# Performance work log

Hardware: AMD Instinct MI355X
Metric: run time of the kernel (lower is better)

## Reference

```python
import jax, jax.numpy as jnp
import numpy as np

N, A, MO, LX, H, S, P, B, BL = 64, 128, 126, 96, 1024, 32, 2, 16, 32
T = (B - 2) * BL
L = B * BL        # 512
IN = MO + A + LX + S      # 382: cat([mo, aud, lxm, style])
GIN = IN + H              # 1406: GRU input = cat([in_embed, mo, aud, lxm, style])

def gelu(x):
    return jax.nn.gelu(x, approximate=False)  # torch F.gelu default (erf)

def gru_cell(x, h, wih, whh, bih, bhh):
    # torch nn.GRU cell math
    gi = x @ wih + bih  # [N,3H]
    gh = h @ whh + bhh  # [N,3H]
    ir, iz, inn = jnp.split(gi, 3, axis=-1)
    hr, hz, hn = jnp.split(gh, 3, axis=-1)
    r = jax.nn.sigmoid(ir + hr)
    z = jax.nn.sigmoid(iz + hz)
    n = jnp.tanh(inn + r * hn)
    return (1.0 - z) * n + z * h

def layernorm(x, g, b, eps=1e-5):
    m = x.mean(-1, keepdims=True)
    v = x.var(-1, keepdims=True)
    return (x - m) * jax.lax.rsqrt(v + eps) * g + b

def setup_inputs():
    key = jax.random.key(0)
    k = jax.random.split(key, 20)
    f = jnp.float32
    def rn(i, shape, s=0.05):
        return jax.random.normal(k[i], shape, dtype=f) * s
    return dict(
        aud_embed=jax.random.normal(k[0], (N, A, T), f),
        mo=jax.random.normal(k[1], (N, MO, L), f),
        lxm=jax.random.normal(k[2], (N, LX, B), f),
        vid_indices=jax.random.randint(k[3], (N, B), 0, 5),
        eps=jax.random.normal(k[4], (T, N, S), f),
        csi_w0=rn(5, (MO + LX, H)), csi_b0=jnp.zeros((H,), f),
        csi_w1=rn(6, (H, H)), csi_b1=jnp.zeros((H,), f),
        csi_w2=rn(7, (H, H * P)), csi_b2=jnp.zeros((H * P,), f),
        spk_emb=rn(8, (5, S), 0.001),
        mu_w=rn(9, (S, S)), mu_b=jnp.zeros((S,), f),
        lv_w=rn(10, (S, S)), lv_b=jnp.zeros((S,), f),
        emb_in_w=rn(11, (IN, H)), emb_in_b=jnp.zeros((H,), f),
        wih0=rn(12, (GIN, 3 * H)), whh0=rn(13, (H, 3 * H)),
        bih0=jnp.zeros((3 * H,), f), bhh0=jnp.zeros((3 * H,), f),
        wih1=rn(14, (H, 3 * H)), whh1=rn(15, (H, 3 * H)),
        bih1=jnp.zeros((3 * H,), f), bhh1=jnp.zeros((3 * H,), f),
        ln_g=jnp.ones((H,), f), ln_b=jnp.zeros((H,), f),
        pred_w=rn(16, (H, MO), 0.02), pred_b=jnp.zeros((MO,), f),
    )

def reference(aud_embed, mo, lxm, vid_indices, eps,
              csi_w0, csi_b0, csi_w1, csi_b1, csi_w2, csi_b2,
              spk_emb, mu_w, mu_b, lv_w, lv_b,
              emb_in_w, emb_in_b,
              wih0, whh0, bih0, bhh0, wih1, whh1, bih1, bhh1,
              ln_g, ln_b, pred_w, pred_b):
    # CellStateInitializer(mo[:,:,BL-1], lxm[:,:,0]) -> [P, N, H]
    x = gelu(jnp.concatenate([mo[:, :, BL - 1], lxm[:, :, 0]], axis=-1) @ csi_w0 + csi_b0)
    x = gelu(x @ csi_w1 + csi_b1)
    x = (x @ csi_w2 + csi_b2).reshape(N, P, H)
    cell = jnp.transpose(x, (1, 0, 2))  # [P,N,H]

    blk = jnp.repeat(jnp.arange(B - 2), BL)            # [T] block index per frame
    aud_seq = jnp.transpose(aud_embed, (2, 0, 1))      # [T,N,A]
    lxm_seq = jnp.transpose(lxm, (2, 0, 1))[blk + 1]   # [T,N,LX]
    vid_seq = vid_indices.T[blk + 1]                   # [T,N]
    zc = spk_emb[vid_seq]                              # [T,N,S]
    z_mu = zc @ mu_w + mu_b                            # [T,N,S]
    z_lv = zc @ lv_w + lv_b                            # [T,N,S]
    style = z_mu + eps * jnp.exp(0.5 * z_lv)           # reparameterize, fresh eps each frame

    def step(carry, xs):
        pre_mo, h0, h1 = carry
        aud_t, lxm_t, st_t = xs
        xcat = jnp.concatenate([pre_mo, aud_t, lxm_t, st_t], axis=-1)  # [N,IN]
        ine = gelu(xcat @ emb_in_w + emb_in_b)                          # [N,H]
        gx = jnp.concatenate([ine, xcat], axis=-1)                      # [N,GIN]
        h0n = gru_cell(gx, h0, wih0, whh0, bih0, bhh0)
        h1n = gru_cell(h0n, h1, wih1, whh1, bih1, bhh1)
        out = layernorm(h1n, ln_g, ln_b)
        pred = out @ pred_w + pred_b                                    # [N,MO]
        return (pred, h0n, h1n), pred

    init = (mo[:, :, BL - 1], cell[0], cell[1])
    _, preds = jax.lax.scan(step, init, (aud_seq, lxm_seq, style))
    mo_hat = jnp.transpose(preds, (1, 2, 0))   # [N,MO,T]
    z_mu_hat = jnp.transpose(z_mu, (1, 2, 0))  # [N,S,T]
    z_lv_hat = jnp.transpose(z_lv, (1, 2, 0))  # [N,S,T]
    return mo_hat, z_mu_hat, z_lv_hat
```

## Files before the change

kernel.cpp:

```cpp
#include <hip/hip_runtime.h>
#include <cmath>

typedef _Float16 f16;
typedef _Float16 f16x8 __attribute__((ext_vector_type(8)));
typedef float f32x4 __attribute__((ext_vector_type(4)));
typedef unsigned long long u64;

#define MFMA_F16(a,b,c) __builtin_amdgcn_mfma_f32_16x16x32_f16((a),(b),(c),0,0,0)
#define AGENT __HIP_MEMORY_SCOPE_AGENT

#define TSTEPS 448
#define OFF_MU 3612672
#define OFF_LV 4530176
#define LDS_BYTES 156160

#define S1 0
#define S2 1
#define S3 2
#define S3B 3
#define S4 4
#define S4G 5

struct Ptrs {
  const float *aud, *mo, *lxm, *eps;
  const int *vid;
  const float *csi_w0, *csi_b0, *csi_w1, *csi_b1, *csi_w2, *csi_b2;
  const float *spk, *mu_w, *mu_b, *lv_w, *lv_b;
  const float *embW, *embB;
  const float *wih0, *whh0, *bih0, *bhh0;
  const float *wih1, *whh1, *bih1, *bhh1;
  const float *ln_g, *ln_b, *predW, *predB;
  float *out;
  unsigned *bar;
  float *mu5, *lv5, *h0F, *h1F, *gsbs;
  f16 *h0B, *h1B, *ineB, *xcat;
  float *ghP0, *ghP1, *x0, *x1, *predsT;
  f16 *whh0P, *whh1P, *wih0aP, *wih0bP, *wih1P, *embWP, *predWP;
};

__device__ __forceinline__ float geluf(float x) {
  return 0.5f * x * (1.0f + erff(x * 0.7071067811865475f));
}
__device__ __forceinline__ float sigmf(float x) {
  return __builtin_amdgcn_rcpf(1.0f + __expf(-x));
}
__device__ __forceinline__ float tanhf_fast(float x) {
  float xc = fmaxf(x, -44.f);
  float e = __expf(-2.f * xc);
  return (1.f - e) * __builtin_amdgcn_rcpf(1.f + e);
}

__device__ __forceinline__ u64 ldc8(const void* p) {
  return __hip_atomic_load((const u64*)p, __ATOMIC_RELAXED, AGENT);
}
__device__ __forceinline__ void stc8(void* p, u64 v) {
  __hip_atomic_store((u64*)p, v, __ATOMIC_RELAXED, AGENT);
}
__device__ __forceinline__ void stcf(float* p, float v) {
  __hip_atomic_store(p, v, __ATOMIC_RELAXED, AGENT);
}
__device__ __forceinline__ f16x8 toH(u64 a, u64 b) {
  union { u64 u[2]; f16x8 h; } r; r.u[0] = a; r.u[1] = b; return r.h;
}
__device__ __forceinline__ f32x4 toF(u64 a, u64 b) {
  union { u64 u[2]; f32x4 f; } r; r.u[0] = a; r.u[1] = b; return r.f;
}
__device__ __forceinline__ u64 packF2(float a, float b) {
  union { float f[2]; u64 u; } r; r.f[0] = a; r.f[1] = b; return r.u;
}
__device__ __forceinline__ void st_pair(f16* base, float v, int lm, bool pred) {
  float vn = __shfl_xor(v, 1);
  if (!(lm & 1) && pred) {
    union { f16 h[2]; unsigned u; } pk;
    pk.h[0] = (f16)v; pk.h[1] = (f16)vn;
    __hip_atomic_store((unsigned*)base, pk.u, __ATOMIC_RELAXED, AGENT);
  }
}


__global__ void k_init(Ptrs p) {
  int gid = blockIdx.x * 256 + threadIdx.x;
  if (gid < 16384) p.bar[gid] = 0u;
}

__global__ void k_pack(const float* __restrict__ src, f16* __restrict__ dst,
                       int K, int rowOff, int realN, int ldN,
                       const float* __restrict__ scale) {
  int ct = blockIdx.x, kt = blockIdx.y;
  int e = threadIdx.x * 2;
  int l = e >> 3, i = e & 7;
  int k = kt * 32 + (l >> 4) * 8 + i;
  int col = ct * 16 + (l & 15);
  f16 v0 = (f16)0.f, v1 = (f16)0.f;
  if (k < K && col < realN) {
    float s = scale ? scale[rowOff + k] : 1.f;
    v0 = (f16)(src[(size_t)(rowOff + k) * ldN + col] * s);
  }
  if (k + 1 < K && col < realN) {
    float s = scale ? scale[rowOff + k + 1] : 1.f;
    v1 = (f16)(src[(size_t)(rowOff + k + 1) * ldN + col] * s);
  }
  size_t o = ((size_t)ct * gridDim.y + kt) * 512 + e;
  dst[o] = v0; dst[o + 1] = v1;
}

__global__ void k_gsbs(Ptrs p) {
  int c = threadIdx.x;
  if (c < 126) {
    float gs = 0.f, bs = 0.f;
    for (int k = 0; k < 1024; k++) {
      float w = p.predW[(size_t)k * 126 + c];
      gs += p.ln_g[k] * w;
      bs += p.ln_b[k] * w;
    }
    p.gsbs[c] = gs; p.gsbs[128 + c] = bs;
  }
}

__global__ void k_csi1(Ptrs p) {
  int gid = blockIdx.x * 256 + threadIdx.x;
  int n = gid >> 10, c = gid & 1023;
  float acc = p.csi_b0[c];
  const float* w = p.csi_w0 + c;
  for (int k = 0; k < 126; k++) acc += p.mo[((size_t)(n * 126 + k)) * 512 + 31] * w[(size_t)k * 1024];
  for (int k = 0; k < 96; k++)  acc += p.lxm[(size_t)(n * 96 + k) * 16] * w[(size_t)(126 + k) * 1024];
  p.x0[gid] = geluf(acc);
}

__global__ void k_csi2(Ptrs p) {
  int gid = blockIdx.x * 256 + threadIdx.x;
  int n = gid >> 10, c = gid & 1023;
  float acc = p.csi_b1[c];
  const float* w = p.csi_w1 + c;
  const float* x = p.x0 + (size_t)n * 1024;
  for (int k = 0; k < 1024; k++) acc += x[k] * w[(size_t)k * 1024];
  p.x1[gid] = geluf(acc);
}

__global__ void k_csi3(Ptrs p) {
  int gid = blockIdx.x * 256 + threadIdx.x;
  int n = gid >> 11, c2 = gid & 2047;
  float acc = p.csi_b2[c2];
  const float* w = p.csi_w2 + c2;
  const float* x = p.x1 + (size_t)n * 1024;
  for (int k = 0; k < 1024; k++) acc += x[k] * w[(size_t)k * 2048];
  if (c2 < 1024) { p.h0F[n * 1024 + c2] = acc; p.h0B[n * 1024 + c2] = (f16)acc; }
  else           { p.h1F[n * 1024 + c2 - 1024] = acc; p.h1B[n * 1024 + c2 - 1024] = (f16)acc; }
}

__global__ void k_gh(Ptrs p) {
  int gid = blockIdx.x * 256 + threadIdx.x;
  int which = gid >= 196608;
  int g2 = which ? gid - 196608 : gid;
  int n = g2 / 3072, c = g2 % 3072;
  const float* h = which ? p.h1F : p.h0F;
  const float* W = which ? p.whh1 : p.whh0;
  const float* bb = which ? p.bhh1 : p.bhh0;
  float acc = bb[c];
  const float* hr = h + (size_t)n * 1024;
  for (int k = 0; k < 1024; k++) acc += hr[k] * W[(size_t)k * 3072 + c];
  int g = c >> 10, col = c & 1023;
  int ct = col >> 4, lm = col & 15, w = n >> 4, lq = (n >> 2) & 3, r = n & 3;
  float* dst = which ? p.ghP1 : p.ghP0;
  dst[((size_t)((ct * 16 + lm) * 16 + w * 4 + lq)) * 16 + g * 4 + r] = acc;
}

__global__ void k_style1(Ptrs p) {
  int tid = threadIdx.x;
  if (tid < 160) {
    int v = tid >> 5, s = tid & 31;
    float m = p.mu_b[s], lv = p.lv_b[s];
    for (int k = 0; k < 32; k++) {
      float z = p.spk[v * 32 + k];
      m += z * p.mu_w[k * 32 + s];
      lv += z * p.lv_w[k * 32 + s];
    }
    p.mu5[v * 32 + s] = m; p.lv5[v * 32 + s] = lv;
  }
}

__global__ void k_style2(Ptrs p) {
  int gid = blockIdx.x * 256 + threadIdx.x;
  int t = gid % 448;
  int rr = gid / 448;
  int s = rr & 31, n = rr >> 5;
  int v = p.vid[n * 16 + (t >> 5) + 1];
  float mu = p.mu5[v * 32 + s], lv = p.lv5[v * 32 + s];
  float e = p.eps[((size_t)t * 64 + n) * 32 + s];
  float st = mu + e * expf(0.5f * lv);
  p.out[OFF_MU + ((size_t)n * 32 + s) * 448 + t] = mu;
  p.out[OFF_LV + ((size_t)n * 32 + s) * 448 + t] = lv;
  p.xcat[((size_t)t * 64 + n) * 384 + 350 + s] = (f16)st;
}

__global__ void k_aud(Ptrs p) {
  __shared__ float tile[32][65];
  int bid = blockIdx.x;
  int n = bid / 28, rem = bid % 28;
  int a0 = (rem / 7) * 32, t0 = (rem % 7) * 64;
  int tid = threadIdx.x;
  for (int i = tid; i < 2048; i += 256) {
    int ai = i >> 6, tj = i & 63;
    tile[ai][tj] = p.aud[((size_t)n * 128 + a0 + ai) * 448 + t0 + tj];
  }
  __syncthreads();
  for (int i = tid; i < 2048; i += 256) {
    int tj = i >> 5, ai = i & 31;
    p.xcat[((size_t)(t0 + tj) * 64 + n) * 384 + 126 + a0 + ai] = (f16)tile[ai][tj];
  }
}

__global__ void k_lxm(Ptrs p) {
  int gid = blockIdx.x * 256 + threadIdx.x;
  int l_ = gid % 96;
  int r = gid / 96;
  int n = r & 63, t = r >> 6;
  int tb = (t >> 5) + 1;
  p.xcat[((size_t)t * 64 + n) * 384 + 254 + l_] = (f16)p.lxm[((size_t)n * 96 + l_) * 16 + tb];
}

__global__ void k_premo0(Ptrs p) {
  int gid = blockIdx.x * 256 + threadIdx.x;
  if (gid < 8064) {
    int n = gid / 126, m = gid % 126;
    p.xcat[(size_t)n * 384 + m] = (f16)p.mo[((size_t)n * 126 + m) * 512 + 31];
  }
}

__global__ void k_padz(Ptrs p) {
  int gid = blockIdx.x * 256 + threadIdx.x;
  int t = gid >> 7, rem = gid & 127;
  int n = rem >> 1, c = 382 + (rem & 1);
  p.xcat[((size_t)t * 64 + n) * 384 + c] = (f16)0.f;
}


__device__ __forceinline__ void sigc(unsigned* bar, int cls, int idx, unsigned val) {
  asm volatile("s_waitcnt vmcnt(0)" ::: "memory");
  __syncthreads();
  if (threadIdx.x == 0)
    __hip_atomic_store(&bar[(cls * 64 + idx) * 32], val, __ATOMIC_RELAXED, AGENT);
}
__device__ __forceinline__ void waitc(unsigned* bar, int cls, unsigned tgt, int nsig) {
  if (threadIdx.x < (unsigned)nsig) {
    const unsigned* f = &bar[(cls * 64 + threadIdx.x) * 32];
    while (__hip_atomic_load(f, __ATOMIC_RELAXED, AGENT) < tgt) {}
  }
  __syncthreads();
}

__device__ __forceinline__ void gemm3(const f16* aRow, const f16* L, int l,
                                      f32x4& A0, f32x4& A1, f32x4& A2) {
  const f16* w0 = L + l * 8;
  u64 ua[16], ub[16];
  #pragma unroll
  for (int j = 0; j < 8; j++) { ua[2*j] = ldc8(aRow + j * 32); ua[2*j+1] = ldc8(aRow + j * 32 + 4); }
  #pragma unroll
  for (int j = 0; j < 8; j++) { ub[2*j] = ldc8(aRow + 256 + j * 32); ub[2*j+1] = ldc8(aRow + 256 + j * 32 + 4); }
  #pragma unroll
  for (int j = 0; j < 8; j++) {
    f16x8 av = toH(ua[2*j], ua[2*j+1]);
    A0 = MFMA_F16(av, *(const f16x8*)(w0 + j * 512), A0);
    A1 = MFMA_F16(av, *(const f16x8*)(w0 + 16384 + j * 512), A1);
    A2 = MFMA_F16(av, *(const f16x8*)(w0 + 32768 + j * 512), A2);
  }
  #pragma unroll
  for (int j = 0; j < 8; j++) { ua[2*j] = ldc8(aRow + 512 + j * 32); ua[2*j+1] = ldc8(aRow + 512 + j * 32 + 4); }
  #pragma unroll
  for (int j = 0; j < 8; j++) {
    f16x8 av = toH(ub[2*j], ub[2*j+1]);
    int kt = 8 + j;
    A0 = MFMA_F16(av, *(const f16x8*)(w0 + kt * 512), A0);
    A1 = MFMA_F16(av, *(const f16x8*)(w0 + 16384 + kt * 512), A1);
    A2 = MFMA_F16(av, *(const f16x8*)(w0 + 32768 + kt * 512), A2);
  }
  #pragma unroll
  for (int j = 0; j < 8; j++) { ub[2*j] = ldc8(aRow + 768 + j * 32); ub[2*j+1] = ldc8(aRow + 768 + j * 32 + 4); }
  #pragma unroll
  for (int j = 0; j < 8; j++) {
    f16x8 av = toH(ua[2*j], ua[2*j+1]);
    int kt = 16 + j;
    A0 = MFMA_F16(av, *(const f16x8*)(w0 + kt * 512), A0);
    A1 = MFMA_F16(av, *(const f16x8*)(w0 + 16384 + kt * 512), A1);
    A2 = MFMA_F16(av, *(const f16x8*)(w0 + 32768 + kt * 512), A2);
  }
  #pragma unroll
  for (int j = 0; j < 8; j++) {
    f16x8 av = toH(ub[2*j], ub[2*j+1]);
    int kt = 24 + j;
    A0 = MFMA_F16(av, *(const f16x8*)(w0 + kt * 512), A0);
    A1 = MFMA_F16(av, *(const f16x8*)(w0 + 16384 + kt * 512), A1);
    A2 = MFMA_F16(av, *(const f16x8*)(w0 + 32768 + kt * 512), A2);
  }
}

__global__ __launch_bounds__(256, 1) void k_scan(Ptrs p) {
  extern __shared__ char smem[];
  f16* L = (f16*)smem;
  const int b = blockIdx.x, tid = threadIdx.x;
  const int w = tid >> 6, l = tid & 63;
  const int lm = l & 15, lq = l >> 4;

  {
    auto cp = [&](int dstF16, const f16* src, int nF16) {
      uint4* d = (uint4*)smem + (dstF16 >> 3);
      const uint4* s = (const uint4*)src;
      for (int i = tid; i < (nF16 >> 3); i += 256) d[i] = s[i];
    };
    if (b < 64) {
      cp(0,     p.wih0aP + (size_t)b * 16384, 16384);
      cp(16384, p.wih0aP + (size_t)(64 + b) * 16384, 16384);
      cp(32768, p.wih0aP + (size_t)(128 + b) * 16384, 16384);
      cp(49152, p.wih0bP + (size_t)b * 6144, 6144);
      cp(55296, p.wih0bP + (size_t)(64 + b) * 6144, 6144);
      cp(61440, p.wih0bP + (size_t)(128 + b) * 6144, 6144);
    } else if (b < 128) {
      int cb = b - 64;
      cp(0,     p.wih1P + (size_t)cb * 16384, 16384);
      cp(16384, p.wih1P + (size_t)(64 + cb) * 16384, 16384);
      cp(32768, p.wih1P + (size_t)(128 + cb) * 16384, 16384);
      cp(49152, p.embWP + (size_t)cb * 6144, 6144);
      if (cb < 8) cp(55296, p.predWP + (size_t)cb * 16384, 16384);
    } else if (b < 192) {
      int i = b - 128;
      cp(0,     p.whh0P + (size_t)i * 16384, 16384);
      cp(16384, p.whh0P + (size_t)(64 + i) * 16384, 16384);
      cp(32768, p.whh0P + (size_t)(128 + i) * 16384, 16384);
    } else {
      int i = b - 192;
      cp(0,     p.whh1P + (size_t)i * 16384, 16384);
      cp(16384, p.whh1P + (size_t)(64 + i) * 16384, 16384);
      cp(32768, p.whh1P + (size_t)(128 + i) * 16384, 16384);
    }
  }
  float b0r = 0.f, b1r = 0.f, b2r = 0.f, ebr = 0.f, pbr = 0.f;
  float GsR = 0.f, BsR = 0.f;
  float hs[4] = {0.f, 0.f, 0.f, 0.f};
  if (b < 64) {
    int col = b * 16 + lm;
    b0r = p.bih0[col]; b1r = p.bih0[1024 + col]; b2r = p.bih0[2048 + col];
    #pragma unroll
    for (int r = 0; r < 4; r++) hs[r] = p.h0F[(size_t)(w * 16 + lq * 4 + r) * 1024 + col];
  } else if (b < 128) {
    int col = (b - 64) * 16 + lm;
    b0r = p.bih1[col]; b1r = p.bih1[1024 + col]; b2r = p.bih1[2048 + col];
    ebr = p.embB[col];
    #pragma unroll
    for (int r = 0; r < 4; r++) hs[r] = p.h1F[(size_t)(w * 16 + lq * 4 + r) * 1024 + col];
    if (b < 72 && col < 126) {
      pbr = p.predB[col];
      GsR = p.gsbs[col];
      BsR = p.gsbs[128 + col];
    }
  } else if (b < 192) {
    int col = (b - 128) * 16 + lm;
    b0r = p.bhh0[col]; b1r = p.bhh0[1024 + col]; b2r = p.bhh0[2048 + col];
  } else {
    int col = (b - 192) * 16 + lm;
    b0r = p.bhh1[col]; b1r = p.bhh1[1024 + col]; b2r = p.bhh1[2048 + col];
  }
  __syncthreads();

  unsigned* bar = p.bar;

  for (unsigned t = 0; t < TSTEPS; t++) {
    const f16* xc = p.xcat + (size_t)t * 24576;

    if (b < 64) {
      f32x4 a0 = {0,0,0,0}, a1 = {0,0,0,0}, a2 = {0,0,0,0};
      const f16* aB = xc + (w * 16 + lm) * 384 + lq * 8;
      const f16* wl = L + 49152 + l * 8;
      #pragma unroll
      for (int kt = 4; kt < 12; kt++) {
        f16x8 av = *(const f16x8*)(aB + kt * 32);
        a0 = MFMA_F16(av, *(const f16x8*)(wl + kt * 512), a0);
        a1 = MFMA_F16(av, *(const f16x8*)(wl + 6144 + kt * 512), a1);
        a2 = MFMA_F16(av, *(const f16x8*)(wl + 12288 + kt * 512), a2);
      }
      if (t) waitc(bar, S4, t, 8);
      f32x4 gip0, gip1, gip2;
      {
        u64 up[8];
        #pragma unroll
        for (int kt = 0; kt < 4; kt++) { up[2*kt] = ldc8(aB + kt * 32); up[2*kt+1] = ldc8(aB + kt * 32 + 4); }
        #pragma unroll
        for (int kt = 0; kt < 4; kt++) {
          f16x8 av = toH(up[2*kt], up[2*kt+1]);
          a0 = MFMA_F16(av, *(const f16x8*)(wl + kt * 512), a0);
          a1 = MFMA_F16(av, *(const f16x8*)(wl + 6144 + kt * 512), a1);
          a2 = MFMA_F16(av, *(const f16x8*)(wl + 12288 + kt * 512), a2);
        }
        #pragma unroll
        for (int r = 0; r < 4; r++) {
          gip0[r] = a0[r] + b0r; gip1[r] = a1[r] + b1r; gip2[r] = a2[r] + b2r;
        }
      }
      waitc(bar, S3B, t, 64);
      const float* rec = p.ghP0 + ((size_t)((b * 16 + lm) * 16 + w * 4 + lq)) * 16;
      u64 r0 = ldc8(rec), r1 = ldc8(rec + 2), r2 = ldc8(rec + 4);
      u64 r3 = ldc8(rec + 6), r4 = ldc8(rec + 8), r5 = ldc8(rec + 10);
      waitc(bar, S1, t + 1, 64);
      {
        f32x4 A0 = {0,0,0,0}, A1 = {0,0,0,0}, A2 = {0,0,0,0};
        gemm3(p.ineB + (w * 16 + lm) * 1024 + lq * 8, L, l, A0, A1, A2);
        f32x4 g0 = toF(r0, r1), g1 = toF(r2, r3), g2 = toF(r4, r5);
        int col = b * 16 + lm;
        #pragma unroll
        for (int r = 0; r < 4; r++) {
          int row = w * 16 + lq * 4 + r;
          float r_ = sigmf(A0[r] + gip0[r] + g0[r]);
          float z_ = sigmf(A1[r] + gip1[r] + g1[r]);
          float n_ = tanhf_fast(A2[r] + gip2[r] + r_ * g2[r]);
          float hn = (1.f - z_) * n_ + z_ * hs[r];
          hs[r] = hn;
          st_pair(p.h0B + (size_t)row * 1024 + col, hn, lm, true);
        }
      }
      sigc(bar, S2, b, t + 1);
    } else if (b < 128) {
      int cb = b - 64;
      int col = cb * 16 + lm;
      f32x4 acc = {0,0,0,0};
      const f16* aB = xc + (w * 16 + lm) * 384 + lq * 8;
      const f16* wl = L + 49152 + l * 8;
      #pragma unroll
      for (int kt = 4; kt < 12; kt++)
        acc = MFMA_F16(*(const f16x8*)(aB + kt * 32), *(const f16x8*)(wl + kt * 512), acc);
      if (t) waitc(bar, S4, t, 8);
      {
        u64 up[8];
        #pragma unroll
        for (int kt = 0; kt < 4; kt++) { up[2*kt] = ldc8(aB + kt * 32); up[2*kt+1] = ldc8(aB + kt * 32 + 4); }
        #pragma unroll
        for (int kt = 0; kt < 4; kt++)
          acc = MFMA_F16(toH(up[2*kt], up[2*kt+1]), *(const f16x8*)(wl + kt * 512), acc);
        #pragma unroll
        for (int r = 0; r < 4; r++) {
          int row = w * 16 + lq * 4 + r;
          float v = geluf(acc[r] + ebr);
          st_pair(p.ineB + (size_t)row * 1024 + col, v, lm, true);
        }
      }
      sigc(bar, S1, cb, t + 1);
      waitc(bar, S4G, t, 64);
      const float* rec = p.ghP1 + ((size_t)((cb * 16 + lm) * 16 + w * 4 + lq)) * 16;
      u64 r0 = ldc8(rec), r1 = ldc8(rec + 2), r2 = ldc8(rec + 4);
      u64 r3 = ldc8(rec + 6), r4 = ldc8(rec + 8), r5 = ldc8(rec + 10);
      waitc(bar, S2, t + 1, 64);
      {
        f32x4 A0 = {0,0,0,0}, A1 = {0,0,0,0}, A2 = {0,0,0,0};
        gemm3(p.h0B + (w * 16 + lm) * 1024 + lq * 8, L, l, A0, A1, A2);
        f32x4 g0 = toF(r0, r1), g1 = toF(r2, r3), g2 = toF(r4, r5);
        #pragma unroll
        for (int r = 0; r < 4; r++) {
          int row = w * 16 + lq * 4 + r;
          float r_ = sigmf(A0[r] + b0r + g0[r]);
          float z_ = sigmf(A1[r] + b1r + g1[r]);
          float n_ = tanhf_fast(A2[r] + b2r + r_ * g2[r]);
          float hn = (1.f - z_) * n_ + z_ * hs[r];
          hs[r] = hn;
          st_pair(p.h1B + (size_t)row * 1024 + col, hn, lm, true);
        }
      }
      sigc(bar, S3, cb, t + 1);
      if (cb < 8) {
        waitc(bar, S3, t + 1, 64);
        int myrow = w * 16 + lm;
        f32x4 pacc = {0,0,0,0};
        const f16* hB = p.h1B + (size_t)myrow * 1024 + lq * 8;
        const f16* wp = L + 55296 + l * 8;
        u64 ua[16], ub[16];
        float ssum = 0.f, ssq = 0.f;
        #pragma unroll
        for (int j = 0; j < 8; j++) { ua[2*j] = ldc8(hB + j * 32); ua[2*j+1] = ldc8(hB + j * 32 + 4); }
        #pragma unroll
        for (int j = 0; j < 8; j++) { ub[2*j] = ldc8(hB + 256 + j * 32); ub[2*j+1] = ldc8(hB + 256 + j * 32 + 4); }
        auto compP = [&](u64* cur, int g) {
          #pragma unroll
          for (int j = 0; j < 8; j++) {
            int kt = g * 8 + j;
            f16x8 hv = toH(cur[2*j], cur[2*j+1]);
            pacc = MFMA_F16(hv, *(const f16x8*)(wp + kt * 512), pacc);
            #pragma unroll
            for (int e = 0; e < 8; e++) {
              float v = (float)hv[e];
              ssum += v; ssq += v * v;
            }
          }
        };
        compP(ua, 0);
        #pragma unroll
        for (int j = 0; j < 8; j++) { ua[2*j] = ldc8(hB + 512 + j * 32); ua[2*j+1] = ldc8(hB + 512 + j * 32 + 4); }
        compP(ub, 1);
        #pragma unroll
        for (int j = 0; j < 8; j++) { ub[2*j] = ldc8(hB + 768 + j * 32); ub[2*j+1] = ldc8(hB + 768 + j * 32 + 4); }
        compP(ua, 2);
        compP(ub, 3);
        ssum += __shfl_xor(ssum, 16); ssq += __shfl_xor(ssq, 16);
        ssum += __shfl_xor(ssum, 32); ssq += __shfl_xor(ssq, 32);
        #pragma unroll
        for (int r = 0; r < 4; r++) {
          int row = w * 16 + lq * 4 + r;
          int src = (l & 48) | (lq * 4 + r);
          float ms = __shfl(ssum, src);
          float qs = __shfl(ssq, src);
          float mean = ms * 0.0009765625f;
          float var  = qs * 0.0009765625f - mean * mean;
          float rstd = rsqrtf(var + 1e-5f);
          float v = rstd * (pacc[r] - mean * GsR) + BsR + pbr;
          if (col < 126) stcf(&p.predsT[(size_t)t * 8064 + row * 126 + col], v);
          st_pair(p.xcat + (size_t)(t + 1) * 24576 + row * 384 + col, v, lm,
                  col < 126 && t < 447);
        }
        sigc(bar, S4, cb, t + 1);
      }
    } else if (b < 192) {
      int i = b - 128;
      waitc(bar, S2, t + 1, 64);
      {
        f32x4 A0 = {0,0,0,0}, A1 = {0,0,0,0}, A2 = {0,0,0,0};
        gemm3(p.h0B + (w * 16 + lm) * 1024 + lq * 8, L, l, A0, A1, A2);
        float* rec = p.ghP0 + ((size_t)((i * 16 + lm) * 16 + w * 4 + lq)) * 16;
        stc8(rec,      packF2(A0[0] + b0r, A0[1] + b0r));
        stc8(rec + 2,  packF2(A0[2] + b0r, A0[3] + b0r));
        stc8(rec + 4,  packF2(A1[0] + b1r, A1[1] + b1r));
        stc8(rec + 6,  packF2(A1[2] + b1r, A1[3] + b1r));
        stc8(rec + 8,  packF2(A2[0] + b2r, A2[1] + b2r));
        stc8(rec + 10, packF2(A2[2] + b2r, A2[3] + b2r));
      }
      sigc(bar, S3B, i, t + 1);
    } else {
      int i = b - 192;
      waitc(bar, S3, t + 1, 64);
      {
        f32x4 A0 = {0,0,0,0}, A1 = {0,0,0,0}, A2 = {0,0,0,0};
        gemm3(p.h1B + (w * 16 + lm) * 1024 + lq * 8, L, l, A0, A1, A2);
        float* rec = p.ghP1 + ((size_t)((i * 16 + lm) * 16 + w * 4 + lq)) * 16;
        stc8(rec,      packF2(A0[0] + b0r, A0[1] + b0r));
        stc8(rec + 2,  packF2(A0[2] + b0r, A0[3] + b0r));
        stc8(rec + 4,  packF2(A1[0] + b1r, A1[1] + b1r));
        stc8(rec + 6,  packF2(A1[2] + b1r, A1[3] + b1r));
        stc8(rec + 8,  packF2(A2[0] + b2r, A2[1] + b2r));
        stc8(rec + 10, packF2(A2[2] + b2r, A2[3] + b2r));
      }
      sigc(bar, S4G, i, t + 1);
    }
  }

  waitc(bar, S4, TSTEPS, 8);
  {
    float* trS = (float*)smem;
    for (int g = b; g < 504; g += 256) {
      int p0 = g * 16;
      for (int t0 = 0; t0 < 448; t0 += 16) {
        int tc = tid >> 4, pp = tid & 15;
        trS[tc * 17 + pp] = p.predsT[(size_t)(t0 + tc) * 8064 + p0 + pp];
        __syncthreads();
        p.out[(size_t)(p0 + (tid >> 4)) * 448 + t0 + (tid & 15)] = trS[(tid & 15) * 17 + (tid >> 4)];
        __syncthreads();
      }
    }
  }
}


extern "C" void kernel_launch(void* const* d_in, const int* in_sizes, int n_in,
                              void* d_out, int out_size, void* d_ws, size_t ws_size,
                              hipStream_t stream) {
  Ptrs p;
  p.aud = (const float*)d_in[0];
  p.mo  = (const float*)d_in[1];
  p.lxm = (const float*)d_in[2];
  p.vid = (const int*)d_in[3];
  p.eps = (const float*)d_in[4];
  p.csi_w0 = (const float*)d_in[5];  p.csi_b0 = (const float*)d_in[6];
  p.csi_w1 = (const float*)d_in[7];  p.csi_b1 = (const float*)d_in[8];
  p.csi_w2 = (const float*)d_in[9];  p.csi_b2 = (const float*)d_in[10];
  p.spk  = (const float*)d_in[11];
  p.mu_w = (const float*)d_in[12];   p.mu_b = (const float*)d_in[13];
  p.lv_w = (const float*)d_in[14];   p.lv_b = (const float*)d_in[15];
  p.embW = (const float*)d_in[16];   p.embB = (const float*)d_in[17];
  p.wih0 = (const float*)d_in[18];   p.whh0 = (const float*)d_in[19];
  p.bih0 = (const float*)d_in[20];   p.bhh0 = (const float*)d_in[21];
  p.wih1 = (const float*)d_in[22];   p.whh1 = (const float*)d_in[23];
  p.bih1 = (const float*)d_in[24];   p.bhh1 = (const float*)d_in[25];
  p.ln_g = (const float*)d_in[26];   p.ln_b = (const float*)d_in[27];
  p.predW = (const float*)d_in[28];  p.predB = (const float*)d_in[29];
  p.out = (float*)d_out;

  char* ws = (char*)d_ws;
  size_t off = 0;
  auto al = [&](size_t bytes) -> void* {
    void* r = (void*)(ws + off);
    off += (bytes + 255) & ~(size_t)255;
    return r;
  };
  p.bar    = (unsigned*)al(65536);
  p.mu5    = (float*)al(640);
  p.lv5    = (float*)al(640);
  p.gsbs   = (float*)al(1024);
  p.h0F    = (float*)al(262144);
  p.h1F    = (float*)al(262144);
  p.h0B    = (f16*)al(131072);
  p.h1B    = (f16*)al(131072);
  p.ineB   = (f16*)al(131072);
  p.ghP0   = (float*)al(1048576);
  p.ghP1   = (float*)al(1048576);
  p.x0     = (float*)al(262144);
  p.x1     = (float*)al(262144);
  p.predsT = (float*)al(14450688);
  p.xcat   = (f16*)al(22020096);
  p.whh0P  = (f16*)al(6291456);
  p.whh1P  = (f16*)al(6291456);
  p.wih0aP = (f16*)al(6291456);
  p.wih0bP = (f16*)al(2359296);
  p.wih1P  = (f16*)al(6291456);
  p.embWP  = (f16*)al(786432);
  p.predWP = (f16*)al(262144);

  k_init<<<64, 256, 0, stream>>>(p);

  k_pack<<<dim3(192, 32), 256, 0, stream>>>(p.whh0, p.whh0P, 1024, 0, 3072, 3072, nullptr);
  k_pack<<<dim3(192, 32), 256, 0, stream>>>(p.whh1, p.whh1P, 1024, 0, 3072, 3072, nullptr);
  k_pack<<<dim3(192, 32), 256, 0, stream>>>(p.wih0, p.wih0aP, 1024, 0, 3072, 3072, nullptr);
  k_pack<<<dim3(192, 12), 256, 0, stream>>>(p.wih0, p.wih0bP, 382, 1024, 3072, 3072, nullptr);
  k_pack<<<dim3(192, 32), 256, 0, stream>>>(p.wih1, p.wih1P, 1024, 0, 3072, 3072, nullptr);
  k_pack<<<dim3(64, 12), 256, 0, stream>>>(p.embW, p.embWP, 382, 0, 1024, 1024, nullptr);
  k_pack<<<dim3(8, 32), 256, 0, stream>>>(p.predW, p.predWP, 1024, 0, 126, 126, p.ln_g);

  k_gsbs<<<1, 128, 0, stream>>>(p);
  k_csi1<<<256, 256, 0, stream>>>(p);
  k_csi2<<<256, 256, 0, stream>>>(p);
  k_csi3<<<512, 256, 0, stream>>>(p);
  k_gh<<<1536, 256, 0, stream>>>(p);
  k_style1<<<1, 256, 0, stream>>>(p);
  k_style2<<<3584, 256, 0, stream>>>(p);
  k_aud<<<1792, 256, 0, stream>>>(p);
  k_lxm<<<10752, 256, 0, stream>>>(p);
  k_premo0<<<32, 256, 0, stream>>>(p);
  k_padz<<<224, 256, 0, stream>>>(p);

  k_scan<<<256, 256, LDS_BYTES, stream>>>(p);

  (void)in_sizes; (void)n_in; (void)out_size; (void)ws_size;
}
```

Baseline: 14.37 ms.

## Fold prediction head into next-step input weights to remove serial pred stage

Precomputes combined weights (predW·ln_g composed with the pre_mo rows of wih0 and embW) so the next step's input projection consumes h1 directly, recomputing layernorm statistics inline. This removes the serial pred stage (S4 barrier) from the per-timestep critical path. The pred output itself moves onto the whh1 blocks and runs in parallel with their gh GEMM. The cost is a much larger extra GEMM over K=1024 in the wih0 and emb blocks every step, plus new setup kernels. Folding the weights in fp16 also adds some precision risk.

```diff
diff --git a/kernel.cpp b/kernel.cpp
--- a/kernel.cpp
+++ b/kernel.cpp
@@ -18,8 +18,7 @@
 #define S2 1
 #define S3 2
 #define S3B 3
-#define S4 4
-#define S4G 5
+#define S4G 4
 
 struct Ptrs {
   const float *aud, *mo, *lxm, *eps;
@@ -32,10 +31,10 @@
   const float *ln_g, *ln_b, *predW, *predB;
   float *out;
   unsigned *bar;
-  float *mu5, *lv5, *h0F, *h1F, *gsbs;
+  float *mu5, *lv5, *h0F, *h1F, *gsbs, *g2b2;
   f16 *h0B, *h1B, *ineB, *xcat;
   float *ghP0, *ghP1, *x0, *x1, *predsT;
-  f16 *whh0P, *whh1P, *wih0aP, *wih0bP, *wih1P, *embWP, *predWP;
+  f16 *whh0P, *whh1P, *wih0aP, *wih0bP, *wih1P, *embWP, *predWP, *wcP, *weP;
 };
 
 __device__ __forceinline__ float geluf(float x) {
@@ -115,6 +114,65 @@
     }
     p.gsbs[c] = gs; p.gsbs[128 + c] = bs;
   }
+}
+
+__global__ void k_g2b2(Ptrs p) {
+  int gid = blockIdx.x * 256 + threadIdx.x;
+  if (gid < 3072) {
+    float g2 = 0.f, b2 = 0.f;
+    for (int m = 0; m < 126; m++) {
+      float w = p.wih0[(size_t)(1024 + m) * 3072 + gid];
+      g2 += p.gsbs[m] * w;
+      b2 += (p.gsbs[128 + m] + p.predB[m]) * w;
+    }
+    p.g2b2[gid] = g2; p.g2b2[3072 + gid] = b2;
+  } else if (gid < 4096) {
+    int c = gid - 3072;
+    float g2 = 0.f, b2 = 0.f;
+    for (int m = 0; m < 126; m++) {
+      float w = p.embW[(size_t)m * 1024 + c];
+      g2 += p.gsbs[m] * w;
+      b2 += (p.gsbs[128 + m] + p.predB[m]) * w;
+    }
+    p.g2b2[6144 + c] = g2; p.g2b2[7168 + c] = b2;
+  }
+}
+
+__global__ void k_cwc(Ptrs p) {
+  int gid = blockIdx.x * 256 + threadIdx.x;
+  int e = gid & 511; int rest = gid >> 9;
+  int kt = rest & 31; rest >>= 5;
+  int g = rest % 3; int b = rest / 3;
+  int l = e >> 3, i = e & 7;
+  int k = kt * 32 + (l >> 4) * 8 + i;
+  int col = b * 16 + (l & 15) + g * 1024;
+  float acc = 0.f;
+  const float* prow = p.predW + (size_t)k * 126;
+  const float* wcol = p.wih0 + (size_t)1024 * 3072 + col;
+  for (int m = 0; m < 126; m++) acc += prow[m] * wcol[(size_t)m * 3072];
+  p.wcP[gid] = (f16)(acc * p.ln_g[k]);
+}
+
+__global__ void k_cwe(Ptrs p) {
+  int gid = blockIdx.x * 256 + threadIdx.x;
+  int e = gid & 511; int rest = gid >> 9;
+  int kt = rest & 31; int cb = rest >> 5;
+  int l = e >> 3, i = e & 7;
+  int k = kt * 32 + (l >> 4) * 8 + i;
+  int col = cb * 16 + (l & 15);
+  float acc = 0.f;
+  const float* prow = p.predW + (size_t)k * 126;
+  const float* wcol = p.embW + col;
+  for (int m = 0; m < 126; m++) acc += prow[m] * wcol[(size_t)m * 1024];
+  p.weP[gid] = (f16)(acc * p.ln_g[k]);
+}
+
+__global__ void k_zpred(Ptrs p) {
+  int gid = blockIdx.x * 256 + threadIdx.x;
+  if (gid >= 1802304) return;
+  int c2 = gid % 63; int u = gid / 63;
+  int n = u & 63; int t = (u >> 6) + 1;
+  ((unsigned*)p.xcat)[((size_t)(t * 64 + n)) * 192 + c2] = 0u;
 }
 
 __global__ void k_csi1(Ptrs p) {
@@ -292,6 +350,97 @@
     A1 = MFMA_F16(av, *(const f16x8*)(w0 + 16384 + kt * 512), A1);
     A2 = MFMA_F16(av, *(const f16x8*)(w0 + 32768 + kt * 512), A2);
   }
+}
+
+__device__ __forceinline__ void gemm4s(const f16* aRow, const f16* L, int l,
+                                       f32x4& A0, f32x4& A1, f32x4& A2,
+                                       f32x4& P, float& ssum, float& ssq) {
+  const f16* w0 = L + l * 8;
+  u64 ua[16], ub[16];
+  #pragma unroll
+  for (int j = 0; j < 8; j++) { ua[2*j] = ldc8(aRow + j * 32); ua[2*j+1] = ldc8(aRow + j * 32 + 4); }
+  #pragma unroll
+  for (int j = 0; j < 8; j++) { ub[2*j] = ldc8(aRow + 256 + j * 32); ub[2*j+1] = ldc8(aRow + 256 + j * 32 + 4); }
+  auto rnd = [&](u64* cur, int base) {
+    #pragma unroll
+    for (int j = 0; j < 8; j++) {
+      int kt = base + j;
+      f16x8 av = toH(cur[2*j], cur[2*j+1]);
+      A0 = MFMA_F16(av, *(const f16x8*)(w0 + kt * 512), A0);
+      A1 = MFMA_F16(av, *(const f16x8*)(w0 + 16384 + kt * 512), A1);
+      A2 = MFMA_F16(av, *(const f16x8*)(w0 + 32768 + kt * 512), A2);
+      P  = MFMA_F16(av, *(const f16x8*)(w0 + 49152 + kt * 512), P);
+      #pragma unroll
+      for (int e = 0; e < 8; e++) { float v = (float)av[e]; ssum += v; ssq += v * v; }
+    }
+  };
+  rnd(ua, 0);
+  #pragma unroll
+  for (int j = 0; j < 8; j++) { ua[2*j] = ldc8(aRow + 512 + j * 32); ua[2*j+1] = ldc8(aRow + 512 + j * 32 + 4); }
+  rnd(ub, 8);
+  #pragma unroll
+  for (int j = 0; j < 8; j++) { ub[2*j] = ldc8(aRow + 768 + j * 32); ub[2*j+1] = ldc8(aRow + 768 + j * 32 + 4); }
+  rnd(ua, 16);
+  rnd(ub, 24);
+}
+
+__device__ __forceinline__ void gemmW(const f16* aRow, const f16* wc, int l,
+                                      f32x4& Q0, f32x4& Q1, f32x4& Q2,
+                                      float& ssum, float& ssq) {
+  const f16* w0 = wc + l * 8;
+  u64 ua[16], ub[16];
+  #pragma unroll
+  for (int j = 0; j < 8; j++) { ua[2*j] = ldc8(aRow + j * 32); ua[2*j+1] = ldc8(aRow + j * 32 + 4); }
+  #pragma unroll
+  for (int j = 0; j < 8; j++) { ub[2*j] = ldc8(aRow + 256 + j * 32); ub[2*j+1] = ldc8(aRow + 256 + j * 32 + 4); }
+  auto rnd = [&](u64* cur, int base) {
+    #pragma unroll
+    for (int j = 0; j < 8; j++) {
+      int kt = base + j;
+      f16x8 av = toH(cur[2*j], cur[2*j+1]);
+      Q0 = MFMA_F16(av, *(const f16x8*)(w0 + kt * 512), Q0);
+      Q1 = MFMA_F16(av, *(const f16x8*)(w0 + (32 + kt) * 512), Q1);
+      Q2 = MFMA_F16(av, *(const f16x8*)(w0 + (64 + kt) * 512), Q2);
+      #pragma unroll
+      for (int e = 0; e < 8; e++) { float v = (float)av[e]; ssum += v; ssq += v * v; }
+    }
+  };
+  rnd(ua, 0);
+  #pragma unroll
+  for (int j = 0; j < 8; j++) { ua[2*j] = ldc8(aRow + 512 + j * 32); ua[2*j+1] = ldc8(aRow + 512 + j * 32 + 4); }
+  rnd(ub, 8);
+  #pragma unroll
+  for (int j = 0; j < 8; j++) { ub[2*j] = ldc8(aRow + 768 + j * 32); ub[2*j+1] = ldc8(aRow + 768 + j * 32 + 4); }
+  rnd(ua, 16);
+  rnd(ub, 24);
+}
+
+__device__ __forceinline__ void gemmE(const f16* aRow, const f16* L, int l,
+                                      f32x4& Q, float& ssum, float& ssq) {
+  const f16* w0 = L + 55296 + l * 8;
+  u64 ua[16], ub[16];
+  #pragma unroll
+  for (int j = 0; j < 8; j++) { ua[2*j] = ldc8(aRow + j * 32); ua[2*j+1] = ldc8(aRow + j * 32 + 4); }
+  #pragma unroll
+  for (int j = 0; j < 8; j++) { ub[2*j] = ldc8(aRow + 256 + j * 32); ub[2*j+1] = ldc8(aRow + 256 + j * 32 + 4); }
+  auto rnd = [&](u64* cur, int base) {
+    #pragma unroll
+    for (int j = 0; j < 8; j++) {
+      int kt = base + j;
+      f16x8 av = toH(cur[2*j], cur[2*j+1]);
+      Q = MFMA_F16(av, *(const f16x8*)(w0 + kt * 512), Q);
+      #pragma unroll
+      for (int e = 0; e < 8; e++) { float v = (float)av[e]; ssum += v; ssq += v * v; }
+    }
+  };
+  rnd(ua, 0);
+  #pragma unroll
+  for (int j = 0; j < 8; j++) { ua[2*j] = ldc8(aRow + 512 + j * 32); ua[2*j+1] = ldc8(aRow + 512 + j * 32 + 4); }
+  rnd(ub, 8);
+  #pragma unroll
+  for (int j = 0; j < 8; j++) { ub[2*j] = ldc8(aRow + 768 + j * 32); ub[2*j+1] = ldc8(aRow + 768 + j * 32 + 4); }
+  rnd(ua, 16);
+  rnd(ub, 24);
 }
 
 __global__ __launch_bounds__(256, 1) void k_scan(Ptrs p) {
@@ -320,7 +469,7 @@
       cp(16384, p.wih1P + (size_t)(64 + cb) * 16384, 16384);
       cp(32768, p.wih1P + (size_t)(128 + cb) * 16384, 16384);
       cp(49152, p.embWP + (size_t)cb * 6144, 6144);
-      if (cb < 8) cp(55296, p.predWP + (size_t)cb * 16384, 16384);
+      cp(55296, p.weP + (size_t)cb * 16384, 16384);
     } else if (b < 192) {
       int i = b - 128;
       cp(0,     p.whh0P + (size_t)i * 16384, 16384);
@@ -331,33 +480,38 @@
       cp(0,     p.whh1P + (size_t)i * 16384, 16384);
       cp(16384, p.whh1P + (size_t)(64 + i) * 16384, 16384);
       cp(32768, p.whh1P + (size_t)(128 + i) * 16384, 16384);
+      if (i < 8) cp(49152, p.predWP + (size_t)i * 16384, 16384);
     }
   }
   float b0r = 0.f, b1r = 0.f, b2r = 0.f, ebr = 0.f, pbr = 0.f;
   float GsR = 0.f, BsR = 0.f;
+  float G2_0 = 0.f, G2_1 = 0.f, G2_2 = 0.f, B2_0 = 0.f, B2_1 = 0.f, B2_2 = 0.f;
   float hs[4] = {0.f, 0.f, 0.f, 0.f};
   if (b < 64) {
     int col = b * 16 + lm;
     b0r = p.bih0[col]; b1r = p.bih0[1024 + col]; b2r = p.bih0[2048 + col];
+    G2_0 = p.g2b2[col];        B2_0 = p.g2b2[3072 + col];
+    G2_1 = p.g2b2[1024 + col]; B2_1 = p.g2b2[3072 + 1024 + col];
+    G2_2 = p.g2b2[2048 + col]; B2_2 = p.g2b2[3072 + 2048 + col];
     #pragma unroll
     for (int r = 0; r < 4; r++) hs[r] = p.h0F[(size_t)(w * 16 + lq * 4 + r) * 1024 + col];
   } else if (b < 128) {
     int col = (b - 64) * 16 + lm;
     b0r = p.bih1[col]; b1r = p.bih1[1024 + col]; b2r = p.bih1[2048 + col];
     ebr = p.embB[col];
+    G2_0 = p.g2b2[6144 + col]; B2_0 = p.g2b2[7168 + col];
     #pragma unroll
     for (int r = 0; r < 4; r++) hs[r] = p.h1F[(size_t)(w * 16 + lq * 4 + r) * 1024 + col];
-    if (b < 72 && col < 126) {
-      pbr = p.predB[col];
-      GsR = p.gsbs[col];
-      BsR = p.gsbs[128 + col];
-    }
   } else if (b < 192) {
     int col = (b - 128) * 16 + lm;
     b0r = p.bhh0[col]; b1r = p.bhh0[1024 + col]; b2r = p.bhh0[2048 + col];
   } else {
     int col = (b - 192) * 16 + lm;
     b0r = p.bhh1[col]; b1r = p.bhh1[1024 + col]; b2r = p.bhh1[2048 + col];
+    if (b < 200) {
+      int pc = (b - 192) * 16 + lm;
+      if (pc < 126) { pbr = p.predB[pc]; GsR = p.gsbs[pc]; BsR = p.gsbs[128 + pc]; }
+    }
   }
   __syncthreads();
 
@@ -377,9 +531,28 @@
         a1 = MFMA_F16(av, *(const f16x8*)(wl + 6144 + kt * 512), a1);
         a2 = MFMA_F16(av, *(const f16x8*)(wl + 12288 + kt * 512), a2);
       }
-      if (t) waitc(bar, S4, t, 8);
-      f32x4 gip0, gip1, gip2;
-      {
+      f32x4 q0 = {0,0,0,0}, q1 = {0,0,0,0}, q2 = {0,0,0,0};
+      float mean_[4], rstd_[4];
+      if (t) {
+        f16x8 av3 = *(const f16x8*)(aB + 3 * 32);
+        a0 = MFMA_F16(av3, *(const f16x8*)(wl + 3 * 512), a0);
+        a1 = MFMA_F16(av3, *(const f16x8*)(wl + 6144 + 3 * 512), a1);
+        a2 = MFMA_F16(av3, *(const f16x8*)(wl + 12288 + 3 * 512), a2);
+        waitc(bar, S3, t, 64);
+        float ssum = 0.f, ssq = 0.f;
+        gemmW(p.h1B + (w * 16 + lm) * 1024 + lq * 8, p.wcP + (size_t)b * 49152,
+              l, q0, q1, q2, ssum, ssq);
+        ssum += __shfl_xor(ssum, 16); ssq += __shfl_xor(ssq, 16);
+        ssum += __shfl_xor(ssum, 32); ssq += __shfl_xor(ssq, 32);
+        #pragma unroll
+        for (int r = 0; r < 4; r++) {
+          int src = (l & 48) | (lq * 4 + r);
+          float ms = __shfl(ssum, src), qs = __shfl(ssq, src);
+          float mean = ms * 0.0009765625f;
+          float var  = qs * 0.0009765625f - mean * mean;
+          mean_[r] = mean; rstd_[r] = rsqrtf(var + 1e-5f);
+        }
+      } else {
         u64 up[8];
         #pragma unroll
         for (int kt = 0; kt < 4; kt++) { up[2*kt] = ldc8(aB + kt * 32); up[2*kt+1] = ldc8(aB + kt * 32 + 4); }
@@ -390,8 +563,16 @@
           a1 = MFMA_F16(av, *(const f16x8*)(wl + 6144 + kt * 512), a1);
           a2 = MFMA_F16(av, *(const f16x8*)(wl + 12288 + kt * 512), a2);
         }
-        #pragma unroll
-        for (int r = 0; r < 4; r++) {
+      }
+      f32x4 gip0, gip1, gip2;
+      #pragma unroll
+      for (int r = 0; r < 4; r++) {
+        if (t) {
+          float rs = rstd_[r], rm = rstd_[r] * mean_[r];
+          gip0[r] = a0[r] + b0r + rs * q0[r] - rm * G2_0 + B2_0;
+          gip1[r] = a1[r] + b1r + rs * q1[r] - rm * G2_1 + B2_1;
+          gip2[r] = a2[r] + b2r + rs * q2[r] - rm * G2_2 + B2_2;
+        } else {
           gip0[r] = a0[r] + b0r; gip1[r] = a1[r] + b1r; gip2[r] = a2[r] + b2r;
         }
       }
@@ -426,20 +607,39 @@
       #pragma unroll
       for (int kt = 4; kt < 12; kt++)
         acc = MFMA_F16(*(const f16x8*)(aB + kt * 32), *(const f16x8*)(wl + kt * 512), acc);
-      if (t) waitc(bar, S4, t, 8);
-      {
+      f32x4 qe = {0,0,0,0};
+      float mean_[4], rstd_[4];
+      if (t) {
+        f16x8 av3 = *(const f16x8*)(aB + 3 * 32);
+        acc = MFMA_F16(av3, *(const f16x8*)(wl + 3 * 512), acc);
+        waitc(bar, S3, t, 64);
+        float ssum = 0.f, ssq = 0.f;
+        gemmE(p.h1B + (w * 16 + lm) * 1024 + lq * 8, L, l, qe, ssum, ssq);
+        ssum += __shfl_xor(ssum, 16); ssq += __shfl_xor(ssq, 16);
+        ssum += __shfl_xor(ssum, 32); ssq += __shfl_xor(ssq, 32);
+        #pragma unroll
+        for (int r = 0; r < 4; r++) {
+          int src = (l & 48) | (lq * 4 + r);
+          float ms = __shfl(ssum, src), qs = __shfl(ssq, src);
+          float mean = ms * 0.0009765625f;
+          float var  = qs * 0.0009765625f - mean * mean;
+          mean_[r] = mean; rstd_[r] = rsqrtf(var + 1e-5f);
+        }
+      } else {
         u64 up[8];
         #pragma unroll
         for (int kt = 0; kt < 4; kt++) { up[2*kt] = ldc8(aB + kt * 32); up[2*kt+1] = ldc8(aB + kt * 32 + 4); }
         #pragma unroll
         for (int kt = 0; kt < 4; kt++)
           acc = MFMA_F16(toH(up[2*kt], up[2*kt+1]), *(const f16x8*)(wl + kt * 512), acc);
-        #pragma unroll
-        for (int r = 0; r < 4; r++) {
-          int row = w * 16 + lq * 4 + r;
-          float v = geluf(acc[r] + ebr);
-          st_pair(p.ineB + (size_t)row * 1024 + col, v, lm, true);
-        }
+      }
+      #pragma unroll
+      for (int r = 0; r < 4; r++) {
+        int row = w * 16 + lq * 4 + r;
+        float pre = acc[r] + ebr;
+        if (t) pre += rstd_[r] * qe[r] - rstd_[r] * mean_[r] * G2_0 + B2_0;
+        float v = geluf(pre);
+        st_pair(p.ineB + (size_t)row * 1024 + col, v, lm, true);
       }
       sigc(bar, S1, cb, t + 1);
       waitc(bar, S4G, t, 64);
@@ -463,57 +663,6 @@
         }
       }
       sigc(bar, S3, cb, t + 1);
-      if (cb < 8) {
-        waitc(bar, S3, t + 1, 64);
-        int myrow = w * 16 + lm;
-        f32x4 pacc = {0,0,0,0};
-        const f16* hB = p.h1B + (size_t)myrow * 1024 + lq * 8;
-        const f16* wp = L + 55296 + l * 8;
-        u64 ua[16], ub[16];
-        float ssum = 0.f, ssq = 0.f;
-        #pragma unroll
-        for (int j = 0; j < 8; j++) { ua[2*j] = ldc8(hB + j * 32); ua[2*j+1] = ldc8(hB + j * 32 + 4); }
-        #pragma unroll
-        for (int j = 0; j < 8; j++) { ub[2*j] = ldc8(hB + 256 + j * 32); ub[2*j+1] = ldc8(hB + 256 + j * 32 + 4); }
-        auto compP = [&](u64* cur, int g) {
-          #pragma unroll
-          for (int j = 0; j < 8; j++) {
-            int kt = g * 8 + j;
-            f16x8 hv = toH(cur[2*j], cur[2*j+1]);
-            pacc = MFMA_F16(hv, *(const f16x8*)(wp + kt * 512), pacc);
-            #pragma unroll
-            for (int e = 0; e < 8; e++) {
-              float v = (float)hv[e];
-              ssum += v; ssq += v * v;
-            }
-          }
-        };
-        compP(ua, 0);
-        #pragma unroll
-        for (int j = 0; j < 8; j++) { ua[2*j] = ldc8(hB + 512 + j * 32); ua[2*j+1] = ldc8(hB + 512 + j * 32 + 4); }
-        compP(ub, 1);
-        #pragma unroll
-        for (int j = 0; j < 8; j++) { ub[2*j] = ldc8(hB + 768 + j * 32); ub[2*j+1] = ldc8(hB + 768 + j * 32 + 4); }
-        compP(ua, 2);
-        compP(ub, 3);
-        ssum += __shfl_xor(ssum, 16); ssq += __shfl_xor(ssq, 16);
-        ssum += __shfl_xor(ssum, 32); ssq += __shfl_xor(ssq, 32);
-        #pragma unroll
-        for (int r = 0; r < 4; r++) {
-          int row = w * 16 + lq * 4 + r;
-          int src = (l & 48) | (lq * 4 + r);
-          float ms = __shfl(ssum, src);
-          float qs = __shfl(ssq, src);
-          float mean = ms * 0.0009765625f;
-          float var  = qs * 0.0009765625f - mean * mean;
-          float rstd = rsqrtf(var + 1e-5f);
-          float v = rstd * (pacc[r] - mean * GsR) + BsR + pbr;
-          if (col < 126) stcf(&p.predsT[(size_t)t * 8064 + row * 126 + col], v);
-          st_pair(p.xcat + (size_t)(t + 1) * 24576 + row * 384 + col, v, lm,
-                  col < 126 && t < 447);
-        }
-        sigc(bar, S4, cb, t + 1);
-      }
     } else if (b < 192) {
       int i = b - 128;
       waitc(bar, S2, t + 1, 64);
@@ -532,9 +681,14 @@
     } else {
       int i = b - 192;
       waitc(bar, S3, t + 1, 64);
+      f32x4 A0 = {0,0,0,0}, A1 = {0,0,0,0}, A2 = {0,0,0,0};
+      f32x4 P = {0,0,0,0};
+      float ssum = 0.f, ssq = 0.f;
+      if (i < 8)
+        gemm4s(p.h1B + (w * 16 + lm) * 1024 + lq * 8, L, l, A0, A1, A2, P, ssum, ssq);
+      else
+        gemm3(p.h1B + (w * 16 + lm) * 1024 + lq * 8, L, l, A0, A1, A2);
       {
-        f32x4 A0 = {0,0,0,0}, A1 = {0,0,0,0}, A2 = {0,0,0,0};
-        gemm3(p.h1B + (w * 16 + lm) * 1024 + lq * 8, L, l, A0, A1, A2);
         float* rec = p.ghP1 + ((size_t)((i * 16 + lm) * 16 + w * 4 + lq)) * 16;
         stc8(rec,      packF2(A0[0] + b0r, A0[1] + b0r));
         stc8(rec + 2,  packF2(A0[2] + b0r, A0[3] + b0r));
@@ -543,11 +697,29 @@
         stc8(rec + 8,  packF2(A2[0] + b2r, A2[1] + b2r));
         stc8(rec + 10, packF2(A2[2] + b2r, A2[3] + b2r));
       }
+      if (i < 8) {
+        ssum += __shfl_xor(ssum, 16); ssq += __shfl_xor(ssq, 16);
+        ssum += __shfl_xor(ssum, 32); ssq += __shfl_xor(ssq, 32);
+        int pc = i * 16 + lm;
+        #pragma unroll
+        for (int r = 0; r < 4; r++) {
+          int src = (l & 48) | (lq * 4 + r);
+          float ms = __shfl(ssum, src), qs = __shfl(ssq, src);
+          float mean = ms * 0.0009765625f;
+          float var  = qs * 0.0009765625f - mean * mean;
+          float rstd = rsqrtf(var + 1e-5f);
+          if (pc < 126) {
+            int row = w * 16 + lq * 4 + r;
+            stcf(&p.predsT[(size_t)t * 8064 + row * 126 + pc],
+                 rstd * (P[r] - mean * GsR) + BsR + pbr);
+          }
+        }
+      }
       sigc(bar, S4G, i, t + 1);
     }
   }
 
-  waitc(bar, S4, TSTEPS, 8);
+  waitc(bar, S4G, TSTEPS, 64);
   {
     float* trS = (float*)smem;
     for (int g = b; g < 504; g += 256) {
@@ -599,6 +771,7 @@
   p.mu5    = (float*)al(640);
   p.lv5    = (float*)al(640);
   p.gsbs   = (float*)al(1024);
+  p.g2b2   = (float*)al(32768);
   p.h0F    = (float*)al(262144);
   p.h1F    = (float*)al(262144);
   p.h0B    = (f16*)al(131072);
@@ -617,6 +790,8 @@
   p.wih1P  = (f16*)al(6291456);
   p.embWP  = (f16*)al(786432);
   p.predWP = (f16*)al(262144);
+  p.wcP    = (f16*)al(6291456);
+  p.weP    = (f16*)al(2097152);
 
   k_init<<<64, 256, 0, stream>>>(p);
 
@@ -629,6 +804,10 @@
   k_pack<<<dim3(8, 32), 256, 0, stream>>>(p.predW, p.predWP, 1024, 0, 126, 126, p.ln_g);
 
   k_gsbs<<<1, 128, 0, stream>>>(p);
+  k_g2b2<<<16, 256, 0, stream>>>(p);
+  k_cwc<<<12288, 256, 0, stream>>>(p);
+  k_cwe<<<4096, 256, 0, stream>>>(p);
+
   k_csi1<<<256, 256, 0, stream>>>(p);
   k_csi2<<<256, 256, 0, stream>>>(p);
   k_csi3<<<512, 256, 0, stream>>>(p);
@@ -639,6 +818,7 @@
   k_lxm<<<10752, 256, 0, stream>>>(p);
   k_premo0<<<32, 256, 0, stream>>>(p);
   k_padz<<<224, 256, 0, stream>>>(p);
+  k_zpred<<<7041, 256, 0, stream>>>(p);
 
   k_scan<<<256, 256, LDS_BYTES, stream>>>(p);
 
```

New measurement: 17.72 ms. +23.3%, slower.
